# Kernel tuning notes

Measured on AMD Instinct MI355X. Metric: run time of the kernel, lower is better.

Reference implementation:

```python
import jax, jax.numpy as jnp
import numpy as np

TOPK = 8
EXTRA = 0  # ADDITIONAL_LAYERS_IN_GPU
CPU_TOPK = int(0.25 * 64)  # CPU_MOE_RATIO * num_experts = 16


def setup_inputs() -> dict:
    key = jax.random.key(0)
    k1, k2 = jax.random.split(key)
    hidden_states = jax.random.normal(k1, (4, 4096, 4096), dtype=jnp.float32)
    wg_weight = jax.random.normal(k2, (64, 4096), dtype=jnp.float32) * 0.02
    return {"hidden_states": hidden_states, "wg_weight": wg_weight}


def reference(hidden_states, wg_weight):
    bsz, seq_len, hidden_size = hidden_states.shape
    x = hidden_states.reshape(-1, hidden_size).astype(jnp.float32)  # [T, H]
    logits = jnp.einsum('th,eh->te', x, wg_weight)  # [T, 64]
    gates = jax.nn.softmax(logits, axis=1)
    values_all, indices_all = jax.lax.top_k(gates, TOPK + EXTRA)
    expert_weight = values_all[:, :TOPK]
    expert_index = indices_all[:, :TOPK]
    _, cpu_expert_index = jax.lax.top_k(gates, CPU_TOPK)
    cpu_expert_index = cpu_expert_index[:, 8 + EXTRA:]
    # norm_topk_prob=True, topk > 1
    eps = jnp.finfo(jnp.float32).eps
    denom = jnp.maximum(expert_weight.sum(axis=1, keepdims=True), eps)
    expert_weight = expert_weight / denom
    return (expert_weight, expert_index, cpu_expert_index, indices_all)
```

## Files before the change

kernel.cpp:

```cpp
#include <hip/hip_runtime.h>

#define T_TOK 16384
#define HDIM  4096
#define NEXP  64
#define TAU   2e-4f
#define BM    128

typedef unsigned short u16;
typedef u16   u16x8  __attribute__((ext_vector_type(8)));
typedef __bf16 bf16x8 __attribute__((ext_vector_type(8)));
typedef float f32x4  __attribute__((ext_vector_type(4)));

__device__ __forceinline__ void gld16(const void* g, void* l) {
    __builtin_amdgcn_global_load_lds(
        (const __attribute__((address_space(1))) void*)g,
        (__attribute__((address_space(3))) void*)l, 16, 0, 0);
}

__global__ __launch_bounds__(256)
void wsplit_kernel(const float* __restrict__ w, u16x8* __restrict__ wfrag,
                   float4* __restrict__ wt4, int* __restrict__ counter) {
    if (blockIdx.x == 0 && threadIdx.x == 0) counter[0] = 0;

    const int id  = blockIdx.x * 256 + threadIdx.x;
    const int e   = id >> 9;
    const int k8g = id & 511;
    const int k   = k8g * 8;

    const float* wp = w + (size_t)e * HDIM + k;
    const float4 v0 = *(const float4*)wp;
    const float4 v1 = *(const float4*)(wp + 4);

    wt4[(size_t)(2 * k8g) * NEXP + e]     = v0;
    wt4[(size_t)(2 * k8g + 1) * NEXP + e] = v1;

    const float fv[8] = {v0.x, v0.y, v0.z, v0.w, v1.x, v1.y, v1.z, v1.w};
    bf16x8 hv, lv;
#pragma unroll
    for (int j = 0; j < 8; ++j) {
        const __bf16 h = (__bf16)fv[j];
        hv[j] = h;
        lv[j] = (__bf16)(fv[j] - (float)h);
    }
    const int chunk = k >> 6;
    const int k8 = (k >> 3) & 7, ks = k8 >> 2, g = k8 & 3, nt = e >> 4;
    const int U = ks * 256 + nt * 64 + 16 * g + (e & 15);
    wfrag[(size_t)chunk * 1024 + U]       = __builtin_bit_cast(u16x8, hv);
    wfrag[(size_t)chunk * 1024 + 512 + U] = __builtin_bit_cast(u16x8, lv);
}

__global__ __launch_bounds__(256, 3)
void gate_gemm_mfma(const float* __restrict__ x, const u16x8* __restrict__ wfrag,
                    float* __restrict__ partial, int ksplit) {
    const int b      = blockIdx.x;
    const int kslice = b % ksplit;
    const int tblk   = b / ksplit;
    const int kspan  = HDIM / ksplit;
    const int k0     = kslice * kspan;
    const int t0     = tblk * BM;
    const int nch    = kspan >> 5;

    __shared__ __align__(16) unsigned char smem[48 * 1024];

    const int tid  = threadIdx.x;
    const int lane = tid & 63;
    const int wv   = tid >> 6;

    f32x4 acc[2][4];
#pragma unroll
    for (int m = 0; m < 2; ++m)
#pragma unroll
        for (int nt = 0; nt < 4; ++nt) acc[m][nt] = (f32x4){0.f, 0.f, 0.f, 0.f};

    auto stage = [&](int c, int p) {
        const int kc  = k0 + (c << 5);
        const u16x8* wsrc = wfrag + (size_t)(kc >> 6) * 1024 + ((c & 1) << 8);
        unsigned char* base = smem + (size_t)p * 1536 * 16;
        gld16(wsrc + tid,       base + (size_t)tid * 16);
        gld16(wsrc + 512 + tid, base + (size_t)(256 + tid) * 16);
#pragma unroll
        for (int j = 0; j < 4; ++j) {
            const int u   = tid + 256 * j;
            const int row = u >> 3;
            const int k4l = (u & 7) ^ (row & 7);
            gld16(x + (size_t)(t0 + row) * HDIM + kc + 4 * k4l,
                  base + (size_t)(512 + u) * 16);
        }
    };

    stage(0, 0);
    __syncthreads();

    for (int c = 0; c < nch; ++c) {
        const int p = c & 1;
        if (c + 1 < nch) stage(c + 1, p ^ 1);

        const u16x8* wb = (const u16x8*)(smem + (size_t)p * 1536 * 16);
        const float* xb = (const float*)(smem + ((size_t)p * 1536 + 512) * 16);
        const int k8 = lane >> 4;

        bf16x8 axh[2], axl[2];
#pragma unroll
        for (int m = 0; m < 2; ++m) {
            const int row = (wv * 2 + m) * 16 + (lane & 15);
            const int p0  = row * 8 + ((2 * k8)     ^ (row & 7));
            const int p1  = row * 8 + ((2 * k8 + 1) ^ (row & 7));
            const float4 va = *(const float4*)(xb + 4 * p0);
            const float4 vb = *(const float4*)(xb + 4 * p1);
            const float fv[8] = {va.x, va.y, va.z, va.w, vb.x, vb.y, vb.z, vb.w};
            bf16x8 hv, lv;
#pragma unroll
            for (int j = 0; j < 8; ++j) {
                const __bf16 h = (__bf16)fv[j];
                hv[j] = h;
                lv[j] = (__bf16)(fv[j] - (float)h);
            }
            axh[m] = hv;
            axl[m] = lv;
        }
#pragma unroll
        for (int nt = 0; nt < 4; ++nt) {
            const bf16x8 bh = __builtin_bit_cast(bf16x8, wb[nt * 64 + lane]);
            const bf16x8 bl = __builtin_bit_cast(bf16x8, wb[256 + nt * 64 + lane]);
#pragma unroll
            for (int m = 0; m < 2; ++m) {
                acc[m][nt] = __builtin_amdgcn_mfma_f32_16x16x32_bf16(axh[m], bh, acc[m][nt], 0, 0, 0);
                acc[m][nt] = __builtin_amdgcn_mfma_f32_16x16x32_bf16(axh[m], bl, acc[m][nt], 0, 0, 0);
                acc[m][nt] = __builtin_amdgcn_mfma_f32_16x16x32_bf16(axl[m], bh, acc[m][nt], 0, 0, 0);
            }
        }
        __syncthreads();
    }

    float* op = partial + (size_t)kslice * T_TOK * NEXP;
    const int ecol = lane & 15;
#pragma unroll
    for (int m = 0; m < 2; ++m) {
        const int trow = t0 + (wv * 2 + m) * 16 + ((lane >> 4) << 2);
#pragma unroll
        for (int nt = 0; nt < 4; ++nt)
#pragma unroll
            for (int r = 0; r < 4; ++r)
                op[(size_t)(trow + r) * NEXP + nt * 16 + ecol] = acc[m][nt][r];
    }
}

__global__ __launch_bounds__(256)
void gate_topk_f32(const float* __restrict__ partial, int ksplit,
                   float* __restrict__ out, int* __restrict__ list,
                   int* __restrict__ counter) {
    const int wave = threadIdx.x >> 6;
    const int lane = threadIdx.x & 63;
    const int t = blockIdx.x * 4 + wave;

    float l = 0.f;
    for (int s = 0; s < ksplit; ++s)
        l += partial[(size_t)s * T_TOK * NEXP + (size_t)t * NEXP + lane];

    float v = l;
    const int idx = lane;
    float myval = -3.4e38f;
    int   myidx = 0;
#pragma unroll
    for (int r = 0; r < 17; ++r) {
        float bv = v;
        int   bi = idx;
#pragma unroll
        for (int s = 1; s < 64; s <<= 1) {
            const float ov = __shfl_xor(bv, s);
            const int   oi = __shfl_xor(bi, s);
            if (ov > bv || (ov == bv && oi < bi)) { bv = ov; bi = oi; }
        }
        if (lane == r) { myval = bv; myidx = bi; }
        if (idx == bi) v = -3.4e38f;
    }

    const float nxt = __shfl(myval, (lane + 1) & 63);
    const bool close = (lane < 16) && (myval - nxt < TAU);
    if (__ballot(close) != 0ull) {
        if (lane == 0) { const int p = atomicAdd(counter, 1); list[p] = t; }
    }

    const float m = __shfl(myval, 0);
    const float p = (lane < 16) ? expf(myval - m) : 0.f;
    float s8 = (lane < 8) ? p : 0.f;
#pragma unroll
    for (int s = 1; s < 64; s <<= 1) s8 += __shfl_xor(s8, s);

    float* ew = out;
    float* ei = out + (size_t)T_TOK * 8;
    float* ci = out + (size_t)2 * T_TOK * 8;
    float* ia = out + (size_t)3 * T_TOK * 8;
    if (lane < 8) {
        ew[(size_t)t * 8 + lane] = p / s8;
        ei[(size_t)t * 8 + lane] = (float)myidx;
        ia[(size_t)t * 8 + lane] = (float)myidx;
    } else if (lane < 16) {
        ci[(size_t)t * 8 + (lane - 8)] = (float)myidx;
    }
}

__global__ __launch_bounds__(256)
void repair_partial(const float* __restrict__ x, const float4* __restrict__ wt4,
                    const int* __restrict__ list, const int* __restrict__ counter,
                    double* __restrict__ fpart) {
    const int lane = threadIdx.x & 63;
    const int wid  = (int)((blockIdx.x * blockDim.x + threadIdx.x) >> 6);
    const int nw   = (int)((gridDim.x * blockDim.x) >> 6);
    const int nit  = counter[0] * 16;

    for (int it = wid; it < nit; it += nw) {
        const int li = it >> 4;
        const int ks = it & 15;
        const int t  = __builtin_amdgcn_readfirstlane(list[li]);
        const float4* xr4 = (const float4*)(x + (size_t)t * HDIM) + ks * 64;
        const float4* wb  = wt4 + (size_t)ks * 64 * NEXP;

        double a0 = 0.0, a1 = 0.0, a2 = 0.0, a3 = 0.0;
#pragma unroll 4
        for (int j = 0; j < 64; j += 4) {
            const float4 w0 = wb[(size_t)(j + 0) * NEXP + lane];
            const float4 w1 = wb[(size_t)(j + 1) * NEXP + lane];
            const float4 w2 = wb[(size_t)(j + 2) * NEXP + lane];
            const float4 w3 = wb[(size_t)(j + 3) * NEXP + lane];
            const float4 x0 = xr4[j + 0];
            const float4 x1 = xr4[j + 1];
            const float4 x2 = xr4[j + 2];
            const float4 x3 = xr4[j + 3];
            a0 = fma((double)x0.x, (double)w0.x, a0);
            a0 = fma((double)x0.y, (double)w0.y, a0);
            a0 = fma((double)x0.z, (double)w0.z, a0);
            a0 = fma((double)x0.w, (double)w0.w, a0);
            a1 = fma((double)x1.x, (double)w1.x, a1);
            a1 = fma((double)x1.y, (double)w1.y, a1);
            a1 = fma((double)x1.z, (double)w1.z, a1);
            a1 = fma((double)x1.w, (double)w1.w, a1);
            a2 = fma((double)x2.x, (double)w2.x, a2);
            a2 = fma((double)x2.y, (double)w2.y, a2);
            a2 = fma((double)x2.z, (double)w2.z, a2);
            a2 = fma((double)x2.w, (double)w2.w, a2);
            a3 = fma((double)x3.x, (double)w3.x, a3);
            a3 = fma((double)x3.y, (double)w3.y, a3);
            a3 = fma((double)x3.z, (double)w3.z, a3);
            a3 = fma((double)x3.w, (double)w3.w, a3);
        }
        fpart[(size_t)li * 1024 + ks * 64 + lane] = (a0 + a1) + (a2 + a3);
    }
}

__global__ __launch_bounds__(256)
void repair_final(const double* __restrict__ fpart, const int* __restrict__ list,
                  const int* __restrict__ counter, float* __restrict__ out) {
    const int lane = threadIdx.x & 63;
    const int wid  = (int)((blockIdx.x * blockDim.x + threadIdx.x) >> 6);
    const int nw   = (int)((gridDim.x * blockDim.x) >> 6);
    const int n    = counter[0];

    for (int li = wid; li < n; li += nw) {
        const int t = __builtin_amdgcn_readfirstlane(list[li]);

        double v = 0.0;
#pragma unroll
        for (int ks = 0; ks < 16; ++ks)
            v += fpart[(size_t)li * 1024 + ks * 64 + lane];

        const int idx = lane;
        double mylog = -1.0e308;
        int    myidx = 0;
#pragma unroll
        for (int r = 0; r < 16; ++r) {
            double bv = v;
            int    bi = idx;
#pragma unroll
            for (int s = 1; s < 64; s <<= 1) {
                const double ov = __shfl_xor(bv, s);
                const int    oi = __shfl_xor(bi, s);
                if (ov > bv || (ov == bv && oi < bi)) { bv = ov; bi = oi; }
            }
            if (lane == r) { mylog = bv; myidx = bi; }
            if (idx == bi) v = -1.0e308;
        }

        const double m = __shfl(mylog, 0);
        const float p = (lane < 16) ? expf((float)(mylog - m)) : 0.f;
        float s8 = (lane < 8) ? p : 0.f;
#pragma unroll
        for (int s = 1; s < 64; s <<= 1) s8 += __shfl_xor(s8, s);

        float* ew = out;
        float* ei = out + (size_t)T_TOK * 8;
        float* ci = out + (size_t)2 * T_TOK * 8;
        float* ia = out + (size_t)3 * T_TOK * 8;
        if (lane < 8) {
            ew[(size_t)t * 8 + lane] = p / s8;
            ei[(size_t)t * 8 + lane] = (float)myidx;
            ia[(size_t)t * 8 + lane] = (float)myidx;
        } else if (lane < 16) {
            ci[(size_t)t * 8 + (lane - 8)] = (float)myidx;
        }
    }
}

extern "C" void kernel_launch(void* const* d_in, const int* in_sizes, int n_in,
                              void* d_out, int out_size, void* d_ws, size_t ws_size,
                              hipStream_t stream) {
    const float* x = (const float*)d_in[0];
    const float* w = (const float*)d_in[1];
    float* out     = (float*)d_out;

    const size_t slice      = (size_t)T_TOK * NEXP * sizeof(float);
    const size_t wfragBytes = (size_t)64 * 1024 * 16;
    const size_t wt4Bytes   = (size_t)NEXP * HDIM * sizeof(float);
    const size_t fpartBytes = (size_t)T_TOK * 16 * NEXP * sizeof(double);
    const size_t extra      = wfragBytes + wt4Bytes + fpartBytes +
                              (size_t)T_TOK * sizeof(int) + 64;

    int ksplit = 1;
    if      (ws_size >= 8 * slice + extra) ksplit = 8;
    else if (ws_size >= 4 * slice + extra) ksplit = 4;
    else if (ws_size >= 2 * slice + extra) ksplit = 2;

    float*  partial = (float*)d_ws;
    u16x8*  wfrag   = (u16x8*)((char*)d_ws + (size_t)ksplit * slice);
    float4* wt4     = (float4*)((char*)wfrag + wfragBytes);
    double* fpart   = (double*)((char*)wt4 + wt4Bytes);
    int*    list    = (int*)((char*)fpart + fpartBytes);
    int*    counter = list + T_TOK;

    wsplit_kernel<<<128, 256, 0, stream>>>(w, wfrag, wt4, counter);
    gate_gemm_mfma<<<ksplit * (T_TOK / BM), 256, 0, stream>>>(x, wfrag, partial, ksplit);
    gate_topk_f32<<<T_TOK / 4, 256, 0, stream>>>(partial, ksplit, out, list, counter);
    repair_partial<<<4096, 256, 0, stream>>>(x, wt4, list, counter, fpart);
    repair_final<<<1024, 256, 0, stream>>>(fpart, list, counter, out);
}
```

Measured before the change: 159.5 us.

## Restructure gate GEMM into 16-token tiles over full K without split-K

The gate GEMM now gives each block 16 tokens and the full 4096-wide reduction. Each wave owns 16 experts and reads its weight fragments straight from global memory instead of staging them in LDS. This drops the split-K partial buffers and the summation step in the top-k kernel, and shrinks LDS so more blocks fit per CU. In exchange, the split bf16 conversion of x is now repeated by all four waves, and weight reloads from L2 rise with the larger block count.

```diff
diff --git a/kernel.cpp b/kernel.cpp
--- a/kernel.cpp
+++ b/kernel.cpp
@@ -4,7 +4,6 @@
 #define HDIM  4096
 #define NEXP  64
 #define TAU   2e-4f
-#define BM    128
 
 typedef unsigned short u16;
 typedef u16   u16x8  __attribute__((ext_vector_type(8)));
@@ -49,64 +48,57 @@
     wfrag[(size_t)chunk * 1024 + 512 + U] = __builtin_bit_cast(u16x8, lv);
 }
 
-__global__ __launch_bounds__(256, 3)
+__global__ __launch_bounds__(256, 5)
 void gate_gemm_mfma(const float* __restrict__ x, const u16x8* __restrict__ wfrag,
-                    float* __restrict__ partial, int ksplit) {
-    const int b      = blockIdx.x;
-    const int kslice = b % ksplit;
-    const int tblk   = b / ksplit;
-    const int kspan  = HDIM / ksplit;
-    const int k0     = kslice * kspan;
-    const int t0     = tblk * BM;
-    const int nch    = kspan >> 5;
-
-    __shared__ __align__(16) unsigned char smem[48 * 1024];
+                    float* __restrict__ logits) {
+    const int t0 = blockIdx.x * 16;
+
+    __shared__ __align__(16) unsigned char smem[32 * 1024];
 
     const int tid  = threadIdx.x;
     const int lane = tid & 63;
     const int wv   = tid >> 6;
 
-    f32x4 acc[2][4];
-#pragma unroll
-    for (int m = 0; m < 2; ++m)
-#pragma unroll
-        for (int nt = 0; nt < 4; ++nt) acc[m][nt] = (f32x4){0.f, 0.f, 0.f, 0.f};
+    f32x4 acc = (f32x4){0.f, 0.f, 0.f, 0.f};
 
     auto stage = [&](int c, int p) {
-        const int kc  = k0 + (c << 5);
-        const u16x8* wsrc = wfrag + (size_t)(kc >> 6) * 1024 + ((c & 1) << 8);
-        unsigned char* base = smem + (size_t)p * 1536 * 16;
-        gld16(wsrc + tid,       base + (size_t)tid * 16);
-        gld16(wsrc + 512 + tid, base + (size_t)(256 + tid) * 16);
+        const int kc = c << 8;
+        unsigned char* base = smem + (size_t)p * 16384;
 #pragma unroll
         for (int j = 0; j < 4; ++j) {
-            const int u   = tid + 256 * j;
-            const int row = u >> 3;
-            const int k4l = (u & 7) ^ (row & 7);
-            gld16(x + (size_t)(t0 + row) * HDIM + kc + 4 * k4l,
-                  base + (size_t)(512 + u) * 16);
+            const int u  = tid + 256 * j;
+            const int r  = u >> 6;
+            const int pj = u & 63;
+            gld16(x + (size_t)(t0 + r) * HDIM + kc + 4 * (pj ^ (r & 7)),
+                  base + (size_t)u * 16);
         }
     };
 
     stage(0, 0);
     __syncthreads();
 
-    for (int c = 0; c < nch; ++c) {
+    for (int c = 0; c < HDIM / 256; ++c) {
         const int p = c & 1;
-        if (c + 1 < nch) stage(c + 1, p ^ 1);
-
-        const u16x8* wb = (const u16x8*)(smem + (size_t)p * 1536 * 16);
-        const float* xb = (const float*)(smem + ((size_t)p * 1536 + 512) * 16);
-        const int k8 = lane >> 4;
-
-        bf16x8 axh[2], axl[2];
-#pragma unroll
-        for (int m = 0; m < 2; ++m) {
-            const int row = (wv * 2 + m) * 16 + (lane & 15);
-            const int p0  = row * 8 + ((2 * k8)     ^ (row & 7));
-            const int p1  = row * 8 + ((2 * k8 + 1) ^ (row & 7));
-            const float4 va = *(const float4*)(xb + 4 * p0);
-            const float4 vb = *(const float4*)(xb + 4 * p1);
+        if (c + 1 < HDIM / 256) stage(c + 1, p ^ 1);
+
+        u16x8 bfh[8], bfl[8];
+        const size_t cb = (size_t)c * 4096;
+#pragma unroll
+        for (int ks = 0; ks < 8; ++ks) {
+            const size_t u = cb + (size_t)(ks >> 1) * 1024 + (ks & 1) * 256
+                           + wv * 64 + lane;
+            bfh[ks] = wfrag[u];
+            bfl[ks] = wfrag[u + 512];
+        }
+
+        const float* xb = (const float*)(smem + (size_t)p * 16384);
+        const int r  = lane & 15;
+        const int rs = r & 7;
+#pragma unroll
+        for (int ks = 0; ks < 8; ++ks) {
+            const int ju = ks * 8 + 2 * (lane >> 4);
+            const float4 va = *(const float4*)(xb + 4 * ((r << 6) + (ju ^ rs)));
+            const float4 vb = *(const float4*)(xb + 4 * ((r << 6) + ((ju + 1) ^ rs)));
             const float fv[8] = {va.x, va.y, va.z, va.w, vb.x, vb.y, vb.z, vb.w};
             bf16x8 hv, lv;
 #pragma unroll
@@ -115,47 +107,29 @@
                 hv[j] = h;
                 lv[j] = (__bf16)(fv[j] - (float)h);
             }
-            axh[m] = hv;
-            axl[m] = lv;
-        }
-#pragma unroll
-        for (int nt = 0; nt < 4; ++nt) {
-            const bf16x8 bh = __builtin_bit_cast(bf16x8, wb[nt * 64 + lane]);
-            const bf16x8 bl = __builtin_bit_cast(bf16x8, wb[256 + nt * 64 + lane]);
-#pragma unroll
-            for (int m = 0; m < 2; ++m) {
-                acc[m][nt] = __builtin_amdgcn_mfma_f32_16x16x32_bf16(axh[m], bh, acc[m][nt], 0, 0, 0);
-                acc[m][nt] = __builtin_amdgcn_mfma_f32_16x16x32_bf16(axh[m], bl, acc[m][nt], 0, 0, 0);
-                acc[m][nt] = __builtin_amdgcn_mfma_f32_16x16x32_bf16(axl[m], bh, acc[m][nt], 0, 0, 0);
-            }
+            acc = __builtin_amdgcn_mfma_f32_16x16x32_bf16(hv, bfh[ks], acc, 0, 0, 0);
+            acc = __builtin_amdgcn_mfma_f32_16x16x32_bf16(hv, bfl[ks], acc, 0, 0, 0);
+            acc = __builtin_amdgcn_mfma_f32_16x16x32_bf16(lv, bfh[ks], acc, 0, 0, 0);
         }
         __syncthreads();
     }
 
-    float* op = partial + (size_t)kslice * T_TOK * NEXP;
-    const int ecol = lane & 15;
-#pragma unroll
-    for (int m = 0; m < 2; ++m) {
-        const int trow = t0 + (wv * 2 + m) * 16 + ((lane >> 4) << 2);
-#pragma unroll
-        for (int nt = 0; nt < 4; ++nt)
-#pragma unroll
-            for (int r = 0; r < 4; ++r)
-                op[(size_t)(trow + r) * NEXP + nt * 16 + ecol] = acc[m][nt][r];
-    }
+    const int trow = t0 + ((lane >> 4) << 2);
+    const int ecol = wv * 16 + (lane & 15);
+#pragma unroll
+    for (int i = 0; i < 4; ++i)
+        logits[(size_t)(trow + i) * NEXP + ecol] = acc[i];
 }
 
 __global__ __launch_bounds__(256)
-void gate_topk_f32(const float* __restrict__ partial, int ksplit,
+void gate_topk_f32(const float* __restrict__ logits,
                    float* __restrict__ out, int* __restrict__ list,
                    int* __restrict__ counter) {
     const int wave = threadIdx.x >> 6;
     const int lane = threadIdx.x & 63;
     const int t = blockIdx.x * 4 + wave;
 
-    float l = 0.f;
-    for (int s = 0; s < ksplit; ++s)
-        l += partial[(size_t)s * T_TOK * NEXP + (size_t)t * NEXP + lane];
+    const float l = logits[(size_t)t * NEXP + lane];
 
     float v = l;
     const int idx = lane;
@@ -308,28 +282,21 @@
     const float* w = (const float*)d_in[1];
     float* out     = (float*)d_out;
 
-    const size_t slice      = (size_t)T_TOK * NEXP * sizeof(float);
-    const size_t wfragBytes = (size_t)64 * 1024 * 16;
-    const size_t wt4Bytes   = (size_t)NEXP * HDIM * sizeof(float);
-    const size_t fpartBytes = (size_t)T_TOK * 16 * NEXP * sizeof(double);
-    const size_t extra      = wfragBytes + wt4Bytes + fpartBytes +
-                              (size_t)T_TOK * sizeof(int) + 64;
-
-    int ksplit = 1;
-    if      (ws_size >= 8 * slice + extra) ksplit = 8;
-    else if (ws_size >= 4 * slice + extra) ksplit = 4;
-    else if (ws_size >= 2 * slice + extra) ksplit = 2;
-
-    float*  partial = (float*)d_ws;
-    u16x8*  wfrag   = (u16x8*)((char*)d_ws + (size_t)ksplit * slice);
+    const size_t logitsBytes = (size_t)T_TOK * NEXP * sizeof(float);
+    const size_t wfragBytes  = (size_t)64 * 1024 * 16;
+    const size_t wt4Bytes    = (size_t)NEXP * HDIM * sizeof(float);
+    const size_t fpartBytes  = (size_t)T_TOK * 16 * NEXP * sizeof(double);
+
+    float*  logits  = (float*)d_ws;
+    u16x8*  wfrag   = (u16x8*)((char*)d_ws + logitsBytes);
     float4* wt4     = (float4*)((char*)wfrag + wfragBytes);
     double* fpart   = (double*)((char*)wt4 + wt4Bytes);
     int*    list    = (int*)((char*)fpart + fpartBytes);
     int*    counter = list + T_TOK;
 
     wsplit_kernel<<<128, 256, 0, stream>>>(w, wfrag, wt4, counter);
-    gate_gemm_mfma<<<ksplit * (T_TOK / BM), 256, 0, stream>>>(x, wfrag, partial, ksplit);
-    gate_topk_f32<<<T_TOK / 4, 256, 0, stream>>>(partial, ksplit, out, list, counter);
+    gate_gemm_mfma<<<T_TOK / 16, 256, 0, stream>>>(x, wfrag, logits);
+    gate_topk_f32<<<T_TOK / 4, 256, 0, stream>>>(logits, out, list, counter);
     repair_partial<<<4096, 256, 0, stream>>>(x, wt4, list, counter, fpart);
     repair_final<<<1024, 256, 0, stream>>>(fpart, list, counter, out);
 }
```

After: 181.9 us. 14.1% more time.
